# Kernel optimization log

Measured on AMD Instinct MI355X. Metric: run time of the kernel, lower is better.

Reference implementation:

```python
import jax, jax.numpy as jnp
import numpy as np

G = 10            # int(2 / 0.2) BEV grid side
NUM_PILLARS = G * G
INTERVAL = 0.2
BN_EPS = 1e-5


def setup_inputs() -> dict:
    key = jax.random.key(0)
    ks = jax.random.split(key, 8)
    B, N = 8, 20000
    x = jax.random.normal(ks[0], (B, N, 3), dtype=jnp.float32)
    # Linear weights stored as [in, out] (torch Linear applies x @ W.T); no biases.
    W1 = jax.random.normal(ks[1], (6, 32), dtype=jnp.float32) * 0.1
    W2 = jax.random.normal(ks[2], (32, 64), dtype=jnp.float32) * 0.1
    W3 = jax.random.normal(ks[3], (64, 128), dtype=jnp.float32) * 0.1
    W4 = jax.random.normal(ks[4], (256, 768), dtype=jnp.float32) * 0.05
    bn_gamma = jnp.ones((NUM_PILLARS,), dtype=jnp.float32)
    bn_beta = jnp.zeros((NUM_PILLARS,), dtype=jnp.float32)
    return {"x": x, "W1": W1, "W2": W2, "W3": W3, "W4": W4,
            "bn_gamma": bn_gamma, "bn_beta": bn_beta}


def _encode_sample(p, seg, W1, W2, W3, W4):
    # p: [N,3] swapped coords (Z,Y,X); seg: [N] pillar id in [0,100)
    N = p.shape[0]
    counts = jax.ops.segment_sum(jnp.ones((N,), p.dtype), seg, num_segments=NUM_PILLARS)  # [100]
    cent = jax.ops.segment_sum(p, seg, num_segments=NUM_PILLARS) / jnp.maximum(counts, 1.0)[:, None]
    aug = jnp.concatenate([p, p - cent[seg]], axis=-1)          # [N,6]
    h = jax.nn.relu(aug @ W1)
    h = jax.nn.relu(h @ W2)
    h = jax.nn.relu(h @ W3)                                      # [N,128]
    pil = jax.ops.segment_max(h, seg, num_segments=NUM_PILLARS)  # [100,128] (-inf on empty, never gathered)
    h2 = jnp.concatenate([h, pil[seg]], axis=-1)                 # [N,256]
    h2 = jax.nn.relu(h2 @ W4)                                    # [N,768]
    enc = jax.ops.segment_max(h2, seg, num_segments=NUM_PILLARS) # [100,768]
    return jnp.where(counts[:, None] > 0, enc, 0.0)             # empty pillars stay zero


def reference(x, W1, W2, W3, W4, bn_gamma, bn_beta):
    # column swap [Y,Z,X] -> [Z,Y,X]
    pts = jnp.stack([x[..., 1], x[..., 0], x[..., 2]], axis=-1)  # [B,N,3]
    # pillar indices from (Y, X) = swapped cols 1:3
    yx = jnp.clip(pts[..., 1:] + 1.0, 0.0, 1.99)
    idx = jnp.floor(yx / INTERVAL).astype(jnp.int32)             # trunc == floor (non-negative)
    seg = idx[..., 0] * G + idx[..., 1]                          # [B,N], matches flatten(2) order y*10+x
    feat = jax.vmap(lambda p, s: _encode_sample(p, s, W1, W2, W3, W4))(pts, seg)  # [B,100,768]
    # BatchNorm1d(100) in training mode over [B, 100, 768]: stats over dims (0,2)
    mean = feat.mean(axis=(0, 2))
    var = feat.var(axis=(0, 2))  # biased variance, as torch uses for normalization
    out = (feat - mean[None, :, None]) * jax.lax.rsqrt(var + BN_EPS)[None, :, None]
    return out * bn_gamma[None, :, None] + bn_beta[None, :, None]
```

## Files before the change

### kernel.cpp

```cpp
#include <hip/hip_runtime.h>
#include <stdint.h>

#define B_    8
#define N_    20000
#define NPTS  (B_*N_)
#define G_    10
#define NPIL  100
#define NSB   (B_*NPIL)
#define BN_EPS 1e-5f

#define OFF_COUNTS   0
#define OFF_SUMS     3200
#define OFF_STARTS   12800
#define ZERO_BYTES   16320
#define OFF_CENT     19264
#define OFF_SEG      28864
#define OFF_W3BF     668864
#define OFF_W4T      709824
#define OFF_PILBF    1103040
#define OFF_PILW4B   1307840
#define OFF_H3P      3765440
#define WS_NEED      44725440

typedef __attribute__((ext_vector_type(8))) short bf16x8;
typedef __attribute__((ext_vector_type(4))) float f32x4;

typedef const __attribute__((address_space(1))) void gas_void;
typedef __attribute__((address_space(3))) void las_void;

__device__ __forceinline__ void gload_lds16(const void* g, void* l){
    __builtin_amdgcn_global_load_lds((gas_void*)g, (las_void*)l, 16, 0, 0);
}

__device__ __forceinline__ int binidx(float v){
    float t = v + 1.0f;
    t = fminf(fmaxf(t, 0.0f), 1.99f);
    return (int)(t / 0.2f);
}
__device__ __forceinline__ unsigned short f2bf(float f){
    unsigned u = __float_as_uint(f);
    u += 0x7fffu + ((u >> 16) & 1u);
    return (unsigned short)(u >> 16);
}
__device__ __forceinline__ unsigned u16max2(unsigned a, unsigned b){
    unsigned ah=a>>16, bh=b>>16, al=a&0xffffu, bl=b&0xffffu;
    return ((ah>bh?ah:bh)<<16) | (al>bl?al:bl);
}
__device__ __forceinline__ uint4 max16(uint4 a, uint4 b){
    uint4 r; r.x=u16max2(a.x,b.x); r.y=u16max2(a.y,b.y);
    r.z=u16max2(a.z,b.z); r.w=u16max2(a.w,b.w); return r;
}

__global__ __launch_bounds__(256) void kA(const float* __restrict__ x,
                                          int* __restrict__ segrank,
                                          int* __restrict__ counts,
                                          float* __restrict__ sums){
    __shared__ int   lc[NPIL];
    __shared__ float lsum[NPIL*3];
    __shared__ int   lbase[NPIL];
    int tid = threadIdx.x;
    if (tid < NPIL){
        lc[tid] = 0;
        lsum[3*tid] = 0.f; lsum[3*tid+1] = 0.f; lsum[3*tid+2] = 0.f;
    }
    __syncthreads();
    int i0  = blockIdx.x * 625;
    int bat = i0 / N_;
    int sv[3], lrv[3];
    #pragma unroll
    for (int t = 0; t < 3; t++){
        int ii = tid + t*256;
        int i  = i0 + ii;
        sv[t] = -1;
        if (ii < 625){
            float x0 = x[3*i], x1 = x[3*i+1], x2 = x[3*i+2];
            int s = binidx(x0)*G_ + binidx(x2);
            sv[t] = s;
            lrv[t] = atomicAdd(&lc[s], 1);
            atomicAdd(&lsum[s*3+0], x1);
            atomicAdd(&lsum[s*3+1], x0);
            atomicAdd(&lsum[s*3+2], x2);
        }
    }
    __syncthreads();
    if (tid < NPIL){
        int c = lc[tid];
        if (c > 0){
            int sb = bat*NPIL + tid;
            lbase[tid] = atomicAdd(&counts[sb], c);
            atomicAdd(&sums[3*sb+0], lsum[3*tid+0]);
            atomicAdd(&sums[3*sb+1], lsum[3*tid+1]);
            atomicAdd(&sums[3*sb+2], lsum[3*tid+2]);
        }
    }
    __syncthreads();
    #pragma unroll
    for (int t = 0; t < 3; t++){
        if (sv[t] >= 0){
            int i = i0 + tid + t*256;
            segrank[i] = (bat*NPIL + sv[t]) | ((lbase[sv[t]] + lrv[t]) << 10);
        }
    }
}

__global__ __launch_bounds__(1024) void kScan(const int* __restrict__ counts,
                                              int* __restrict__ starts){
    __shared__ int s[1024];
    int t = threadIdx.x;
    int c = (t < NSB) ? counts[t] : 0;
    s[t] = c;
    __syncthreads();
    for (int off=1; off<1024; off<<=1){
        int v = (t >= off) ? s[t-off] : 0;
        __syncthreads();
        s[t] += v;
        __syncthreads();
    }
    if (t < NSB) starts[t] = s[t]-c;
    if (t == NSB) starts[NSB] = s[NSB-1];
}

__global__ __launch_bounds__(256) void kB(const int* __restrict__ counts,
                                          const float* __restrict__ sums,
                                          float* __restrict__ cent,
                                          const float* __restrict__ W3,
                                          unsigned short* __restrict__ W3bf,
                                          const float* __restrict__ W4,
                                          unsigned short* __restrict__ W4T){
    int idx = blockIdx.x*256 + threadIdx.x;
    if (idx < 2400){
        cent[idx] = sums[idx] / fmaxf((float)counts[idx/3], 1.0f);
    } else if (idx < 2400 + 8192){
        int t = idx - 2400;
        int col = t >> 6, k = t & 63;
        W3bf[t] = f2bf(W3[k*128 + col]);
    } else if (idx < 2400 + 8192 + 196608){
        int t = idx - 2400 - 8192;
        int k = t / 768, j = t - k*768;
        W4T[j*256 + k] = f2bf(W4[t]);
    }
}

__global__ __launch_bounds__(256) void kC12(const float* __restrict__ x,
                                            const int* __restrict__ segrank,
                                            const int* __restrict__ starts,
                                            const float* __restrict__ cent,
                                            const float* __restrict__ W1,
                                            const float* __restrict__ W2,
                                            unsigned short* __restrict__ h3p){
    int i = blockIdx.x*256 + threadIdx.x;
    if (i >= NPTS) return;
    int pk = segrank[i];
    int sb = pk & 1023;
    int pos = starts[sb] + (pk >> 10);
    float p0 = x[3*i+1], p1 = x[3*i], p2 = x[3*i+2];
    float aug[6];
    aug[0]=p0; aug[1]=p1; aug[2]=p2;
    aug[3]=p0-cent[sb*3+0]; aug[4]=p1-cent[sb*3+1]; aug[5]=p2-cent[sb*3+2];

    float h1[32];
    #pragma unroll
    for (int j=0;j<32;j++){
        float a = 0.f;
        #pragma unroll
        for (int k=0;k<6;k++) a += aug[k]*W1[k*32+j];
        h1[j] = fmaxf(a, 0.f);
    }
    unsigned buf[32];
    #pragma unroll 8
    for (int jp=0;jp<32;jp++){
        float a0 = 0.f, a1 = 0.f;
        #pragma unroll
        for (int k=0;k<32;k++){
            a0 += h1[k]*W2[k*64 + jp*2];
            a1 += h1[k]*W2[k*64 + jp*2 + 1];
        }
        buf[jp] = (unsigned)f2bf(fmaxf(a0,0.f)) | ((unsigned)f2bf(fmaxf(a1,0.f)) << 16);
    }
    uint4* d4 = (uint4*)(h3p + (size_t)pos*128 + 64);
    #pragma unroll
    for (int q=0;q<8;q++) d4[q] = ((const uint4*)buf)[q];
}

__global__ __launch_bounds__(512) void kC3(const unsigned short* __restrict__ W3bf,
                                           unsigned short* __restrict__ h3p){
    __shared__ unsigned short Al[256*64];
    __shared__ unsigned short Bl[128*64];
    int tid = threadIdx.x;
    int m0  = blockIdx.x * 256;
    #pragma unroll
    for (int it=0; it<4; it++){
        int cc = tid + it*512;
        int row = cc >> 3, ch = cc & 7;
        int chs = ch ^ (row & 7);
        gload_lds16(h3p + (size_t)(m0+row)*128 + 64 + chs*8, (char*)Al + cc*16);
    }
    #pragma unroll
    for (int it=0; it<2; it++){
        int cc = tid + it*512;
        int row = cc >> 3, ch = cc & 7;
        int chs = ch ^ (row & 7);
        gload_lds16(W3bf + (size_t)row*64 + chs*8, (char*)Bl + cc*16);
    }
    __syncthreads();

    int lane = tid & 63, wid = tid >> 6;
    int wm = wid >> 1, wn = wid & 1;
    int l15 = lane & 15, lhi = lane >> 4;

    f32x4 acc[4][4];
    #pragma unroll
    for (int m=0;m<4;m++)
        #pragma unroll
        for (int n=0;n<4;n++) acc[m][n] = (f32x4){0.f,0.f,0.f,0.f};

    #pragma unroll
    for (int kk=0; kk<2; kk++){
        bf16x8 af[4], bfr[4];
        #pragma unroll
        for (int f=0; f<4; f++){
            int ra = wm*64 + f*16 + l15;
            af[f]  = *(const bf16x8*)((char*)Al + ra*128 + (((kk*4+lhi) ^ (ra&7))*16));
            int rb = wn*64 + f*16 + l15;
            bfr[f] = *(const bf16x8*)((char*)Bl + rb*128 + (((kk*4+lhi) ^ (rb&7))*16));
        }
        #pragma unroll
        for (int m=0;m<4;m++)
            #pragma unroll
            for (int n=0;n<4;n++)
                acc[m][n] = __builtin_amdgcn_mfma_f32_16x16x32_bf16(af[m], bfr[n], acc[m][n], 0,0,0);
    }

    #pragma unroll
    for (int m=0;m<4;m++)
        #pragma unroll
        for (int r=0;r<4;r++){
            int row = m0 + wm*64 + m*16 + lhi*4 + r;
            #pragma unroll
            for (int n=0;n<4;n++){
                int col = wn*64 + n*16 + l15;
                h3p[(size_t)row*128 + col] = f2bf(fmaxf(acc[m][n][r], 0.f));
            }
        }
}

__global__ __launch_bounds__(256) void kM(const unsigned short* __restrict__ h3p,
                                          const int* __restrict__ starts,
                                          unsigned short* __restrict__ pilbf){
    __shared__ uint4 sd[16][16];
    int sb = blockIdx.x;
    int tx = threadIdx.x & 15, ty = threadIdx.x >> 4;
    int s = starts[sb], npts = starts[sb+1] - s;
    uint4 acc = {0u,0u,0u,0u};
    for (int p = ty; p < npts; p += 16){
        uint4 v = *(const uint4*)(h3p + (size_t)(s+p)*128 + tx*8);
        acc = max16(acc, v);
    }
    sd[ty][tx] = acc;
    __syncthreads();
    #pragma unroll
    for (int off=8; off; off>>=1){
        if (ty < off) sd[ty][tx] = max16(sd[ty][tx], sd[ty+off][tx]);
        __syncthreads();
    }
    if (ty == 0) *(uint4*)(pilbf + sb*128 + tx*8) = sd[0][tx];
}

__global__ __launch_bounds__(256) void kPB(const unsigned short* __restrict__ pilbf,
                                           const unsigned short* __restrict__ W4T,
                                           float* __restrict__ pilW4b){
    __shared__ unsigned short Al[128*128];
    __shared__ unsigned short Bl[128*128];
    int m0 = blockIdx.x * 128;
    int n0 = blockIdx.y * 128;
    int tid = threadIdx.x;
    #pragma unroll
    for (int it=0; it<8; it++){
        int cc = tid + it*256;
        int row = cc >> 4, ch = cc & 15;
        int chs = ch ^ (row & 15);
        uint4 v = {0u,0u,0u,0u};
        if (m0 + row < NSB) v = *(const uint4*)(pilbf + (size_t)(m0+row)*128 + chs*8);
        *(uint4*)((char*)Al + cc*16) = v;
        uint4 vb = *(const uint4*)(W4T + (size_t)(n0+row)*256 + 128 + chs*8);
        *(uint4*)((char*)Bl + cc*16) = vb;
    }
    __syncthreads();
    int lane = tid & 63, wid = tid >> 6;
    int wm = wid >> 1, wn = wid & 1;
    int l15 = lane & 15, lhi = lane >> 4;
    f32x4 acc[4][4];
    #pragma unroll
    for (int m=0;m<4;m++)
        #pragma unroll
        for (int n=0;n<4;n++) acc[m][n] = (f32x4){0.f,0.f,0.f,0.f};
    #pragma unroll
    for (int kk=0; kk<4; kk++){
        bf16x8 af[4], bfr[4];
        #pragma unroll
        for (int f=0; f<4; f++){
            int ra = wm*64 + f*16 + l15;
            af[f]  = *(const bf16x8*)((char*)Al + ra*256 + (((kk*4+lhi) ^ (ra&15))*16));
            int rb = wn*64 + f*16 + l15;
            bfr[f] = *(const bf16x8*)((char*)Bl + rb*256 + (((kk*4+lhi) ^ (rb&15))*16));
        }
        #pragma unroll
        for (int m=0;m<4;m++)
            #pragma unroll
            for (int n=0;n<4;n++)
                acc[m][n] = __builtin_amdgcn_mfma_f32_16x16x32_bf16(af[m], bfr[n], acc[m][n], 0,0,0);
    }
    #pragma unroll
    for (int m=0;m<4;m++)
        #pragma unroll
        for (int r=0;r<4;r++){
            int p = wm*64 + m*16 + lhi*4 + r;
            int sbp = m0 + p;
            if (sbp < NSB){
                #pragma unroll
                for (int n=0;n<4;n++)
                    pilW4b[(size_t)sbp*768 + n0 + wn*64 + n*16 + l15] = acc[m][n][r];
            }
        }
}

__global__ __launch_bounds__(256) void kD(const unsigned short* __restrict__ h3p,
                                          const int* __restrict__ starts,
                                          const float* __restrict__ pilW4b,
                                          const unsigned short* __restrict__ W4T,
                                          float* __restrict__ out){
    __shared__ unsigned short Al[64*128];
    __shared__ float red[2][2][64];
    int b  = blockIdx.x;
    int x_ = b & 7, t_ = b >> 3;
    int k_ = t_ / 6, nt = t_ - k_*6;
    int sb = x_ + 8*k_;
    int n0 = nt * 128;
    int tid = threadIdx.x;
    int start = starts[sb];
    int npts  = starts[sb+1] - start;
    if (npts == 0){
        if (tid < 128) out[(size_t)sb*768 + n0 + tid] = 0.f;
        return;
    }
    int lane = tid & 63, wid = tid >> 6;
    int wm = wid >> 1, wn = wid & 1;
    int l15 = lane & 15, lhi = lane >> 4;

    bf16x8 bfr[4][4];
    #pragma unroll
    for (int kk=0;kk<4;kk++)
        #pragma unroll
        for (int n=0;n<4;n++){
            int rb = n0 + wn*64 + n*16 + l15;
            bfr[kk][n] = *(const bf16x8*)(W4T + (size_t)rb*256 + (kk*4+lhi)*8);
        }

    const unsigned short* asrc[4];
    int arow[4], achs[4];
    #pragma unroll
    for (int it=0; it<4; it++){
        int cc = tid + it*256;
        int row = cc >> 4, ch = cc & 15;
        arow[it] = row;
        achs[it] = ch ^ (row & 15);
        asrc[it] = h3p + (size_t)(start+row)*128 + achs[it]*8;
    }

    float mx[2][4][4];
    #pragma unroll
    for (int m=0;m<2;m++)
        #pragma unroll
        for (int n=0;n<4;n++)
            #pragma unroll
            for (int r=0;r<4;r++) mx[m][n][r] = -3.0e38f;

    int nfull = npts >> 6;
    int tailr = npts & 63;

    for (int c=0; c<nfull; c++){
        __syncthreads();
        #pragma unroll
        for (int it=0; it<4; it++){
            gload_lds16(asrc[it], (char*)Al + (tid + it*256)*16);
            asrc[it] += 64*128;
        }
        __syncthreads();
        f32x4 acc[2][4];
        #pragma unroll
        for (int m=0;m<2;m++)
            #pragma unroll
            for (int n=0;n<4;n++) acc[m][n] = (f32x4){0.f,0.f,0.f,0.f};
        #pragma unroll
        for (int kk=0; kk<4; kk++){
            bf16x8 af[2];
            #pragma unroll
            for (int f=0; f<2; f++){
                int ra = wm*32 + f*16 + l15;
                af[f] = *(const bf16x8*)((const char*)Al + ra*256 + (((kk*4+lhi) ^ (ra&15))*16));
            }
            #pragma unroll
            for (int m=0;m<2;m++)
                #pragma unroll
                for (int n=0;n<4;n++)
                    acc[m][n] = __builtin_amdgcn_mfma_f32_16x16x32_bf16(af[m], bfr[kk][n], acc[m][n], 0,0,0);
        }
        #pragma unroll
        for (int m=0;m<2;m++)
            #pragma unroll
            for (int n=0;n<4;n++)
                #pragma unroll
                for (int r=0;r<4;r++)
                    mx[m][n][r] = fmaxf(mx[m][n][r], acc[m][n][r]);
    }
    if (tailr > 0){
        int base = nfull << 6;
        __syncthreads();
        #pragma unroll
        for (int it=0; it<4; it++){
            int idx = start + base + arow[it];
            idx = idx < NPTS ? idx : NPTS-1;
            gload_lds16(h3p + (size_t)idx*128 + achs[it]*8, (char*)Al + (tid + it*256)*16);
        }
        __syncthreads();
        f32x4 acc[2][4];
        #pragma unroll
        for (int m=0;m<2;m++)
            #pragma unroll
            for (int n=0;n<4;n++) acc[m][n] = (f32x4){0.f,0.f,0.f,0.f};
        #pragma unroll
        for (int kk=0; kk<4; kk++){
            bf16x8 af[2];
            #pragma unroll
            for (int f=0; f<2; f++){
                int ra = wm*32 + f*16 + l15;
                af[f] = *(const bf16x8*)((const char*)Al + ra*256 + (((kk*4+lhi) ^ (ra&15))*16));
            }
            #pragma unroll
            for (int m=0;m<2;m++)
                #pragma unroll
                for (int n=0;n<4;n++)
                    acc[m][n] = __builtin_amdgcn_mfma_f32_16x16x32_bf16(af[m], bfr[kk][n], acc[m][n], 0,0,0);
        }
        #pragma unroll
        for (int m=0;m<2;m++)
            #pragma unroll
            for (int r=0;r<4;r++){
                int p = wm*32 + m*16 + lhi*4 + r;
                if (p < tailr){
                    #pragma unroll
                    for (int n=0;n<4;n++)
                        mx[m][n][r] = fmaxf(mx[m][n][r], acc[m][n][r]);
                }
            }
    }

    float red4[4];
    #pragma unroll
    for (int n=0;n<4;n++){
        float v = -3.0e38f;
        #pragma unroll
        for (int m=0;m<2;m++)
            #pragma unroll
            for (int r=0;r<4;r++) v = fmaxf(v, mx[m][n][r]);
        v = fmaxf(v, __shfl_xor(v, 16));
        v = fmaxf(v, __shfl_xor(v, 32));
        red4[n] = v;
    }
    if (lhi == 0){
        #pragma unroll
        for (int n=0;n<4;n++) red[wm][wn][n*16 + l15] = red4[n];
    }
    __syncthreads();
    if (wm == 0){
        float v = fmaxf(red[0][wn][lane], red[1][wn][lane]);
        int col = n0 + wn*64 + lane;
        v = fmaxf(v + pilW4b[(size_t)sb*768 + col], 0.f);
        out[(size_t)sb*768 + col] = v;
    }
}

__global__ __launch_bounds__(256) void kE(float* __restrict__ out,
                                          const float* __restrict__ gamma,
                                          const float* __restrict__ beta){
    int p = blockIdx.x;
    int tid = threadIdx.x;
    float v[B_*3];
    float sum = 0.f, ssq = 0.f;
    #pragma unroll
    for (int b=0;b<B_;b++)
        #pragma unroll
        for (int r=0;r<3;r++){
            float t = out[(b*NPIL + p)*768 + tid + r*256];
            v[b*3+r] = t;
            sum += t; ssq += t*t;
        }
    #pragma unroll
    for (int off=32; off; off>>=1){
        sum += __shfl_xor(sum, off);
        ssq += __shfl_xor(ssq, off);
    }
    __shared__ float ls[8];
    __shared__ float sc[2];
    int lane = tid & 63, w = tid >> 6;
    if (lane == 0){ ls[w] = sum; ls[4+w] = ssq; }
    __syncthreads();
    if (tid == 0){
        float S = ls[0]+ls[1]+ls[2]+ls[3];
        float Q = ls[4]+ls[5]+ls[6]+ls[7];
        float mean = S * (1.0f/6144.0f);
        float var  = Q * (1.0f/6144.0f) - mean*mean;
        float scale = rsqrtf(var + BN_EPS) * gamma[p];
        sc[0] = scale;
        sc[1] = beta[p] - mean*scale;
    }
    __syncthreads();
    float scale = sc[0], shift = sc[1];
    #pragma unroll
    for (int b=0;b<B_;b++)
        #pragma unroll
        for (int r=0;r<3;r++)
            out[(b*NPIL + p)*768 + tid + r*256] = v[b*3+r]*scale + shift;
}

extern "C" void kernel_launch(void* const* d_in, const int* in_sizes, int n_in,
                              void* d_out, int out_size, void* d_ws, size_t ws_size,
                              hipStream_t stream){
    if (ws_size < (size_t)WS_NEED) return;
    const float* x     = (const float*)d_in[0];
    const float* W1    = (const float*)d_in[1];
    const float* W2    = (const float*)d_in[2];
    const float* W3    = (const float*)d_in[3];
    const float* W4    = (const float*)d_in[4];
    const float* gamma = (const float*)d_in[5];
    const float* beta  = (const float*)d_in[6];
    float* out = (float*)d_out;
    char*  ws  = (char*)d_ws;

    int*            counts = (int*)           (ws + OFF_COUNTS);
    float*          sums   = (float*)         (ws + OFF_SUMS);
    int*            starts = (int*)           (ws + OFF_STARTS);
    float*          cent   = (float*)         (ws + OFF_CENT);
    int*            segrank= (int*)           (ws + OFF_SEG);
    unsigned short* W3bf   = (unsigned short*)(ws + OFF_W3BF);
    unsigned short* W4T    = (unsigned short*)(ws + OFF_W4T);
    unsigned short* pilbf  = (unsigned short*)(ws + OFF_PILBF);
    float*          pilW4b = (float*)         (ws + OFF_PILW4B);
    unsigned short* h3p    = (unsigned short*)(ws + OFF_H3P);

    hipMemsetAsync(d_ws, 0, ZERO_BYTES, stream);

    kA<<<256, 256, 0, stream>>>(x, segrank, counts, sums);
    kScan<<<1, 1024, 0, stream>>>(counts, starts);
    kB<<<(2400+8192+196608+255)/256, 256, 0, stream>>>(counts, sums, cent, W3, W3bf, W4, W4T);
    kC12<<<(NPTS+255)/256, 256, 0, stream>>>(x, segrank, starts, cent, W1, W2, h3p);
    kC3<<<NPTS/256, 512, 0, stream>>>(W3bf, h3p);
    kM<<<NSB, 256, 0, stream>>>(h3p, starts, pilbf);
    dim3 gPB((NSB+127)/128, 6);
    kPB<<<gPB, 256, 0, stream>>>(pilbf, W4T, pilW4b);
    kD<<<4800, 256, 0, stream>>>(h3p, starts, pilW4b, W4T, out);
    kE<<<NPIL, 256, 0, stream>>>(out, gamma, beta);
}
```

Measured before the change: 196.9 us.

## Stage W4 tile in LDS and process two pillar-segments per kD block

kD now loads its 128x256 W4T slice once into swizzled LDS and has each block handle two sample-pillar segments (sb and sb+400), halving the grid. B fragments are read from LDS per k-step instead of being held in 64 registers for the whole kernel. The aim is to amortise the weight load across segments and free registers for occupancy. The cost is extra LDS reads per MFMA step, a larger LDS footprint, and less parallelism, since work per block is now serialised over two segments.

```diff
diff --git a/kernel.cpp b/kernel.cpp
--- a/kernel.cpp
+++ b/kernel.cpp
@@ -330,153 +330,169 @@
                                           const unsigned short* __restrict__ W4T,
                                           float* __restrict__ out){
     __shared__ unsigned short Al[64*128];
+    __shared__ unsigned short Bl[128*128];
     __shared__ float red[2][2][64];
     int b  = blockIdx.x;
     int x_ = b & 7, t_ = b >> 3;
     int k_ = t_ / 6, nt = t_ - k_*6;
-    int sb = x_ + 8*k_;
+    int sb0 = x_ + 8*k_;
     int n0 = nt * 128;
     int tid = threadIdx.x;
-    int start = starts[sb];
-    int npts  = starts[sb+1] - start;
-    if (npts == 0){
-        if (tid < 128) out[(size_t)sb*768 + n0 + tid] = 0.f;
-        return;
+    #pragma unroll
+    for (int it=0; it<8; it++){
+        int cc = tid + it*256;
+        int row = cc >> 4, ch = cc & 15;
+        int chs = ch ^ (row & 15);
+        gload_lds16(W4T + (size_t)(n0+row)*256 + chs*8, (char*)Bl + cc*16);
+    }
+    int arow[4], achs[4];
+    #pragma unroll
+    for (int it=0; it<4; it++){
+        int cc = tid + it*256;
+        arow[it] = cc >> 4;
+        achs[it] = (cc & 15) ^ (arow[it] & 15);
     }
     int lane = tid & 63, wid = tid >> 6;
     int wm = wid >> 1, wn = wid & 1;
     int l15 = lane & 15, lhi = lane >> 4;
 
-    bf16x8 bfr[4][4];
-    #pragma unroll
-    for (int kk=0;kk<4;kk++)
-        #pragma unroll
-        for (int n=0;n<4;n++){
-            int rb = n0 + wn*64 + n*16 + l15;
-            bfr[kk][n] = *(const bf16x8*)(W4T + (size_t)rb*256 + (kk*4+lhi)*8);
-        }
-
-    const unsigned short* asrc[4];
-    int arow[4], achs[4];
-    #pragma unroll
-    for (int it=0; it<4; it++){
-        int cc = tid + it*256;
-        int row = cc >> 4, ch = cc & 15;
-        arow[it] = row;
-        achs[it] = ch ^ (row & 15);
-        asrc[it] = h3p + (size_t)(start+row)*128 + achs[it]*8;
-    }
-
-    float mx[2][4][4];
-    #pragma unroll
-    for (int m=0;m<2;m++)
-        #pragma unroll
-        for (int n=0;n<4;n++)
-            #pragma unroll
-            for (int r=0;r<4;r++) mx[m][n][r] = -3.0e38f;
-
-    int nfull = npts >> 6;
-    int tailr = npts & 63;
-
-    for (int c=0; c<nfull; c++){
-        __syncthreads();
-        #pragma unroll
-        for (int it=0; it<4; it++){
-            gload_lds16(asrc[it], (char*)Al + (tid + it*256)*16);
-            asrc[it] += 64*128;
-        }
-        __syncthreads();
-        f32x4 acc[2][4];
+    #pragma unroll
+    for (int pp=0; pp<2; pp++){
+        int sb = sb0 + pp*400;
+        int start = starts[sb];
+        int npts  = starts[sb+1] - start;
+        if (npts == 0){
+            __syncthreads();
+            if (tid < 128) out[(size_t)sb*768 + n0 + tid] = 0.f;
+            continue;
+        }
+        const unsigned short* asrc[4];
+        #pragma unroll
+        for (int it=0; it<4; it++)
+            asrc[it] = h3p + (size_t)(start+arow[it])*128 + achs[it]*8;
+
+        float mx[2][4][4];
         #pragma unroll
         for (int m=0;m<2;m++)
             #pragma unroll
-            for (int n=0;n<4;n++) acc[m][n] = (f32x4){0.f,0.f,0.f,0.f};
-        #pragma unroll
-        for (int kk=0; kk<4; kk++){
-            bf16x8 af[2];
-            #pragma unroll
-            for (int f=0; f<2; f++){
-                int ra = wm*32 + f*16 + l15;
-                af[f] = *(const bf16x8*)((const char*)Al + ra*256 + (((kk*4+lhi) ^ (ra&15))*16));
+            for (int n=0;n<4;n++)
+                #pragma unroll
+                for (int r=0;r<4;r++) mx[m][n][r] = -3.0e38f;
+
+        int nfull = npts >> 6;
+        int tailr = npts & 63;
+
+        for (int c=0; c<nfull; c++){
+            __syncthreads();
+            #pragma unroll
+            for (int it=0; it<4; it++){
+                gload_lds16(asrc[it], (char*)Al + (tid + it*256)*16);
+                asrc[it] += 64*128;
             }
+            __syncthreads();
+            f32x4 acc[2][4];
             #pragma unroll
             for (int m=0;m<2;m++)
                 #pragma unroll
-                for (int n=0;n<4;n++)
-                    acc[m][n] = __builtin_amdgcn_mfma_f32_16x16x32_bf16(af[m], bfr[kk][n], acc[m][n], 0,0,0);
-        }
-        #pragma unroll
-        for (int m=0;m<2;m++)
-            #pragma unroll
-            for (int n=0;n<4;n++)
-                #pragma unroll
-                for (int r=0;r<4;r++)
-                    mx[m][n][r] = fmaxf(mx[m][n][r], acc[m][n][r]);
-    }
-    if (tailr > 0){
-        int base = nfull << 6;
-        __syncthreads();
-        #pragma unroll
-        for (int it=0; it<4; it++){
-            int idx = start + base + arow[it];
-            idx = idx < NPTS ? idx : NPTS-1;
-            gload_lds16(h3p + (size_t)idx*128 + achs[it]*8, (char*)Al + (tid + it*256)*16);
-        }
-        __syncthreads();
-        f32x4 acc[2][4];
-        #pragma unroll
-        for (int m=0;m<2;m++)
-            #pragma unroll
-            for (int n=0;n<4;n++) acc[m][n] = (f32x4){0.f,0.f,0.f,0.f};
-        #pragma unroll
-        for (int kk=0; kk<4; kk++){
-            bf16x8 af[2];
-            #pragma unroll
-            for (int f=0; f<2; f++){
-                int ra = wm*32 + f*16 + l15;
-                af[f] = *(const bf16x8*)((const char*)Al + ra*256 + (((kk*4+lhi) ^ (ra&15))*16));
-            }
-            #pragma unroll
-            for (int m=0;m<2;m++)
-                #pragma unroll
-                for (int n=0;n<4;n++)
-                    acc[m][n] = __builtin_amdgcn_mfma_f32_16x16x32_bf16(af[m], bfr[kk][n], acc[m][n], 0,0,0);
-        }
-        #pragma unroll
-        for (int m=0;m<2;m++)
-            #pragma unroll
-            for (int r=0;r<4;r++){
-                int p = wm*32 + m*16 + lhi*4 + r;
-                if (p < tailr){
+                for (int n=0;n<4;n++) acc[m][n] = (f32x4){0.f,0.f,0.f,0.f};
+            #pragma unroll
+            for (int kk=0; kk<4; kk++){
+                bf16x8 af[2], bfr[4];
+                #pragma unroll
+                for (int f=0; f<2; f++){
+                    int ra = wm*32 + f*16 + l15;
+                    af[f] = *(const bf16x8*)((const char*)Al + ra*256 + (((kk*4+lhi) ^ (ra&15))*16));
+                }
+                #pragma unroll
+                for (int f=0; f<4; f++){
+                    int rb = wn*64 + f*16 + l15;
+                    bfr[f] = *(const bf16x8*)((const char*)Bl + rb*256 + (((kk*4+lhi) ^ (rb&15))*16));
+                }
+                #pragma unroll
+                for (int m=0;m<2;m++)
                     #pragma unroll
                     for (int n=0;n<4;n++)
+                        acc[m][n] = __builtin_amdgcn_mfma_f32_16x16x32_bf16(af[m], bfr[n], acc[m][n], 0,0,0);
+            }
+            #pragma unroll
+            for (int m=0;m<2;m++)
+                #pragma unroll
+                for (int n=0;n<4;n++)
+                    #pragma unroll
+                    for (int r=0;r<4;r++)
                         mx[m][n][r] = fmaxf(mx[m][n][r], acc[m][n][r]);
+        }
+        if (tailr > 0){
+            int base = nfull << 6;
+            __syncthreads();
+            #pragma unroll
+            for (int it=0; it<4; it++){
+                int idx = start + base + arow[it];
+                idx = idx < NPTS ? idx : NPTS-1;
+                gload_lds16(h3p + (size_t)idx*128 + achs[it]*8, (char*)Al + (tid + it*256)*16);
+            }
+            __syncthreads();
+            f32x4 acc[2][4];
+            #pragma unroll
+            for (int m=0;m<2;m++)
+                #pragma unroll
+                for (int n=0;n<4;n++) acc[m][n] = (f32x4){0.f,0.f,0.f,0.f};
+            #pragma unroll
+            for (int kk=0; kk<4; kk++){
+                bf16x8 af[2], bfr[4];
+                #pragma unroll
+                for (int f=0; f<2; f++){
+                    int ra = wm*32 + f*16 + l15;
+                    af[f] = *(const bf16x8*)((const char*)Al + ra*256 + (((kk*4+lhi) ^ (ra&15))*16));
                 }
+                #pragma unroll
+                for (int f=0; f<4; f++){
+                    int rb = wn*64 + f*16 + l15;
+                    bfr[f] = *(const bf16x8*)((const char*)Bl + rb*256 + (((kk*4+lhi) ^ (rb&15))*16));
+                }
+                #pragma unroll
+                for (int m=0;m<2;m++)
+                    #pragma unroll
+                    for (int n=0;n<4;n++)
+                        acc[m][n] = __builtin_amdgcn_mfma_f32_16x16x32_bf16(af[m], bfr[n], acc[m][n], 0,0,0);
             }
-    }
-
-    float red4[4];
-    #pragma unroll
-    for (int n=0;n<4;n++){
-        float v = -3.0e38f;
-        #pragma unroll
-        for (int m=0;m<2;m++)
-            #pragma unroll
-            for (int r=0;r<4;r++) v = fmaxf(v, mx[m][n][r]);
-        v = fmaxf(v, __shfl_xor(v, 16));
-        v = fmaxf(v, __shfl_xor(v, 32));
-        red4[n] = v;
-    }
-    if (lhi == 0){
-        #pragma unroll
-        for (int n=0;n<4;n++) red[wm][wn][n*16 + l15] = red4[n];
-    }
-    __syncthreads();
-    if (wm == 0){
-        float v = fmaxf(red[0][wn][lane], red[1][wn][lane]);
-        int col = n0 + wn*64 + lane;
-        v = fmaxf(v + pilW4b[(size_t)sb*768 + col], 0.f);
-        out[(size_t)sb*768 + col] = v;
+            #pragma unroll
+            for (int m=0;m<2;m++)
+                #pragma unroll
+                for (int r=0;r<4;r++){
+                    int p = wm*32 + m*16 + lhi*4 + r;
+                    if (p < tailr){
+                        #pragma unroll
+                        for (int n=0;n<4;n++)
+                            mx[m][n][r] = fmaxf(mx[m][n][r], acc[m][n][r]);
+                    }
+                }
+        }
+
+        float red4[4];
+        #pragma unroll
+        for (int n=0;n<4;n++){
+            float v = -3.0e38f;
+            #pragma unroll
+            for (int m=0;m<2;m++)
+                #pragma unroll
+                for (int r=0;r<4;r++) v = fmaxf(v, mx[m][n][r]);
+            v = fmaxf(v, __shfl_xor(v, 16));
+            v = fmaxf(v, __shfl_xor(v, 32));
+            red4[n] = v;
+        }
+        __syncthreads();
+        if (lhi == 0){
+            #pragma unroll
+            for (int n=0;n<4;n++) red[wm][wn][n*16 + l15] = red4[n];
+        }
+        __syncthreads();
+        if (wm == 0){
+            float v = fmaxf(red[0][wn][lane], red[1][wn][lane]);
+            int col = n0 + wn*64 + lane;
+            v = fmaxf(v + pilW4b[(size_t)sb*768 + col], 0.f);
+            out[(size_t)sb*768 + col] = v;
+        }
     }
 }
 
@@ -558,6 +574,6 @@
     kM<<<NSB, 256, 0, stream>>>(h3p, starts, pilbf);
     dim3 gPB((NSB+127)/128, 6);
     kPB<<<gPB, 256, 0, stream>>>(pilbf, W4T, pilW4b);
-    kD<<<4800, 256, 0, stream>>>(h3p, starts, pilW4b, W4T, out);
+    kD<<<2400, 256, 0, stream>>>(h3p, starts, pilW4b, W4T, out);
     kE<<<NPIL, 256, 0, stream>>>(out, gamma, beta);
 }
```

After: 173.1 us. -12.1%, faster.
